# Kernel optimization log

Hardware: AMD Instinct MI355X
Metric: run time of the kernel (lower is better)

The kernel has to match this reference:

```python
import jax, jax.numpy as jnp
import numpy as np

E = 1024
H = 16
D = E // H  # head_dim = 64


def setup_inputs() -> dict:
    key = jax.random.key(0)
    k_x, k_w1, k_b1, k_w2, k_b2 = jax.random.split(key, 5)
    s = 1.0 / np.sqrt(E)
    return {
        "x": jax.random.normal(k_x, (2, 2048, E), dtype=jnp.float32),
        "qkv_w": jax.random.uniform(k_w1, (3 * E, E), jnp.float32, -s, s),
        "qkv_b": jax.random.uniform(k_b1, (3 * E,), jnp.float32, -s, s),
        "out_w": jax.random.uniform(k_w2, (E, E), jnp.float32, -s, s),
        "out_b": jax.random.uniform(k_b2, (E,), jnp.float32, -s, s),
    }


def reference(x, qkv_w, qkv_b, out_w, out_b):
    B, T, _ = x.shape
    # qkv projection (torch Linear: x @ W.T + b)
    qkv = x @ qkv_w.T + qkv_b  # [B, T, 3E]
    q, k, v = jnp.split(qkv, 3, axis=-1)
    # [B, T, E] -> [B, H, T, D]
    def to_heads(t):
        return t.reshape(B, T, H, D).transpose(0, 2, 1, 3)
    q, k, v = to_heads(q), to_heads(k), to_heads(v)
    scale = 1.0 / np.sqrt(D).astype(np.float32)
    scores = jnp.einsum("bhqd,bhkd->bhqk", q, k) * scale  # [B, H, T, T]
    attn = jax.nn.softmax(scores, axis=-1)
    # dropout is identity in eval mode
    out = jnp.einsum("bhqk,bhkd->bhqd", attn, v)  # [B, H, T, D]
    out = out.transpose(0, 2, 1, 3).reshape(B, T, E)
    return out @ out_w.T + out_b
```

## Files before the change

### kernel.cpp

```cpp
#include <hip/hip_runtime.h>

#define TT 2048
#define BB 2
#define EE 1024
#define HH 16
#define DD 64
#define E3 3072
#define NTOK 4096

typedef unsigned short u16;
typedef _Float16 __attribute__((ext_vector_type(8))) half8;
typedef __attribute__((ext_vector_type(4))) float f32x4;

__device__ __forceinline__ unsigned f2h(float f) {
    union { _Float16 h; u16 u; } v; v.h = (_Float16)f; return (unsigned)v.u;
}

__device__ __forceinline__ void async_ld16(const u16* g, const u16* l) {
    auto gp = reinterpret_cast<const __attribute__((address_space(1))) unsigned*>(
        reinterpret_cast<uintptr_t>(g));
    auto lp = reinterpret_cast<__attribute__((address_space(3))) unsigned*>(
        reinterpret_cast<uintptr_t>(l));
    __builtin_amdgcn_global_load_lds(gp, lp, 16, 0, 0);
}

__global__ __launch_bounds__(256) void split3(
    const float* __restrict__ x, const float* __restrict__ w1,
    const float* __restrict__ w2,
    u16* __restrict__ xh, u16* __restrict__ w1h, u16* __restrict__ w2h)
{
    const int N1 = (NTOK * EE) / 4;
    const int N2 = N1 + (E3 * EE) / 4;
    int i = blockIdx.x * 256 + threadIdx.x;
    const float* src; u16* dst; int j;
    if (i < N1)      { src = x;  dst = xh;  j = i; }
    else if (i < N2) { src = w1; dst = w1h; j = i - N1; }
    else             { src = w2; dst = w2h; j = i - N2; }
    float4 v = ((const float4*)src)[j];
    *(uint2*)&dst[(size_t)j * 4] = make_uint2(
        f2h(v.x) | (f2h(v.y) << 16), f2h(v.z) | (f2h(v.w) << 16));
}

__global__ __launch_bounds__(256) void vtrans(
    const u16* __restrict__ qkv, u16* __restrict__ vt)
{
    __shared__ u16 L[64][72];
    const int tid = threadIdx.x;
    const int t0 = blockIdx.x * 64;
    const int h  = blockIdx.y;
    const int b  = blockIdx.z;
    const int row = tid >> 2;
    const int c16 = (tid & 3) << 4;

    const u16* src = qkv + (size_t)(b * TT + t0 + row) * E3 + 2 * EE + h * DD + c16;
    *(uint4*)&L[row][c16]     = *(const uint4*)src;
    *(uint4*)&L[row][c16 + 8] = *(const uint4*)(src + 8);
    __syncthreads();

    union { uint4 u[2]; u16 s[16]; } P;
#pragma unroll
    for (int j = 0; j < 16; ++j) P.s[j] = L[c16 + j][row];
    u16* dst = vt + ((size_t)(b * HH + h) * DD + row) * TT + t0 + c16;
    *(uint4*)dst       = P.u[0];
    *(uint4*)(dst + 8) = P.u[1];
}

template <int WMT, bool ALO, bool F16OUT>
__global__ __launch_bounds__(256) void gemm_f16(
    const u16* __restrict__ Ahg, const u16* __restrict__ Alg,
    const u16* __restrict__ Whg,
    const float* __restrict__ bias, void* __restrict__ Cout, int M, int N)
{
    constexpr int BM = WMT * 32;
    constexpr int AHALF = BM / 64;
    __shared__ u16 sAh[BM * 32];
    __shared__ u16 sAl[ALO ? BM * 32 : 64];
    __shared__ u16 sBh[128 * 32];

    const int tid  = threadIdx.x;
    const int lane = tid & 63;
    const int wave = tid >> 6;
    const int quad = lane >> 4;
    const int l16  = lane & 15;
    const int wm = wave >> 1, wn = wave & 1;
    const int m0 = blockIdx.y * BM;
    const int n0 = blockIdx.x * 128;

    const u16* agh[AHALF]; const u16* agl[AHALF]; int aldw[AHALF];
#pragma unroll
    for (int h = 0; h < AHALF; ++h) {
        int s = h * 256 + tid;
        int row = s >> 2, k8p = s & 3;
        int k8 = k8p ^ ((row >> 1) & 3);
        agh[h] = Ahg + (size_t)(m0 + row) * EE + k8 * 8;
        agl[h] = ALO ? Alg + (size_t)(m0 + row) * EE + k8 * 8 : nullptr;
        aldw[h] = (h * 256 + wave * 64) * 8;
    }
    const u16* bgh[2]; int bldw[2];
#pragma unroll
    for (int h = 0; h < 2; ++h) {
        int s = h * 256 + tid;
        int row = s >> 2, k8p = s & 3;
        int k8 = k8p ^ ((row >> 1) & 3);
        bgh[h] = Whg + (size_t)(n0 + row) * EE + k8 * 8;
        bldw[h] = (h * 256 + wave * 64) * 8;
    }

    int aoff[WMT], boff[4];
#pragma unroll
    for (int mt = 0; mt < WMT; ++mt) {
        int r = wm * (WMT * 16) + mt * 16 + l16;
        aoff[mt] = r * 32 + (quad ^ ((r >> 1) & 3)) * 8;
    }
#pragma unroll
    for (int nt = 0; nt < 4; ++nt) {
        int r = wn * 64 + nt * 16 + l16;
        boff[nt] = r * 32 + (quad ^ ((r >> 1) & 3)) * 8;
    }

    f32x4 acc[WMT][4];
#pragma unroll
    for (int mt = 0; mt < WMT; ++mt)
#pragma unroll
        for (int nt = 0; nt < 4; ++nt) acc[mt][nt] = (f32x4){0.f, 0.f, 0.f, 0.f};

    for (int k0 = 0; k0 < EE; k0 += 32) {
        __syncthreads();
#pragma unroll
        for (int h = 0; h < AHALF; ++h) {
            async_ld16(agh[h] + k0, sAh + aldw[h]);
            if (ALO) async_ld16(agl[h] + k0, sAl + aldw[h]);
        }
#pragma unroll
        for (int h = 0; h < 2; ++h)
            async_ld16(bgh[h] + k0, sBh + bldw[h]);
        __syncthreads();

        half8 fah[WMT], fal[WMT], fbh[4];
#pragma unroll
        for (int mt = 0; mt < WMT; ++mt) {
            fah[mt] = *(const half8*)&sAh[aoff[mt]];
            if (ALO) fal[mt] = *(const half8*)&sAl[aoff[mt]];
        }
#pragma unroll
        for (int nt = 0; nt < 4; ++nt)
            fbh[nt] = *(const half8*)&sBh[boff[nt]];
#pragma unroll
        for (int mt = 0; mt < WMT; ++mt)
#pragma unroll
            for (int nt = 0; nt < 4; ++nt) {
                f32x4 c = acc[mt][nt];
                if (ALO)
                    c = __builtin_amdgcn_mfma_f32_16x16x32_f16(fal[mt], fbh[nt], c, 0, 0, 0);
                c = __builtin_amdgcn_mfma_f32_16x16x32_f16(fah[mt], fbh[nt], c, 0, 0, 0);
                acc[mt][nt] = c;
            }
    }

    float bv[4];
#pragma unroll
    for (int nt = 0; nt < 4; ++nt) bv[nt] = bias[n0 + wn * 64 + nt * 16 + l16];
#pragma unroll
    for (int mt = 0; mt < WMT; ++mt)
#pragma unroll
        for (int nt = 0; nt < 4; ++nt)
#pragma unroll
            for (int r = 0; r < 4; ++r) {
                int rg = m0 + wm * (WMT * 16) + mt * 16 + quad * 4 + r;
                int cg = n0 + wn * 64 + nt * 16 + l16;
                float v = acc[mt][nt][r] + bv[nt];
                if (F16OUT) ((u16*)Cout)[(size_t)rg * N + cg] = (u16)f2h(v);
                else        ((float*)Cout)[(size_t)rg * N + cg] = v;
            }
}

__global__ __launch_bounds__(256, 3) void attn_mfma(
    const u16* __restrict__ qkv, const u16* __restrict__ vt,
    u16* __restrict__ obuf)
{
    __shared__ u16 KB[2][64][64];
    __shared__ u16 VB[2][64][64];
    __shared__ u16 QP[128][64];

    const int tid  = threadIdx.x;
    const int wave = tid >> 6;
    const int lane = tid & 63;
    const int quad = lane >> 4;
    const int l16  = lane & 15;

    const int q0 = blockIdx.x * 128;
    const int hh = blockIdx.y;
    const int b  = blockIdx.z;
    const float C1 = 0.18033688011112042f;

    const int srow = tid >> 3;
    const int schk = tid & 7;
    const int ldsw = wave * 512;

#pragma unroll
    for (int p = 0; p < 4; ++p) {
        int row = p * 32 + srow;
        const u16* qg = qkv + (size_t)(b * TT + q0 + row) * E3 + hh * DD
                        + ((schk ^ (row & 7)) << 3);
        async_ld16(qg, &QP[0][0] + p * 2048 + ldsw);
    }
#pragma unroll
    for (int p = 0; p < 2; ++p) {
        int row = p * 32 + srow;
        int sw8 = (schk ^ (row & 7)) << 3;
        async_ld16(qkv + (size_t)(b * TT + row) * E3 + EE + hh * DD + sw8,
                   &KB[0][0][0] + p * 2048 + ldsw);
        async_ld16(vt + ((size_t)(b * HH + hh) * DD + row) * TT + sw8,
                   &VB[0][0][0] + p * 2048 + ldsw);
    }
    __syncthreads();

    half8 qb[2][2];
#pragma unroll
    for (int qt = 0; qt < 2; ++qt) {
        int row = wave * 32 + qt * 16 + l16;
#pragma unroll
        for (int ks = 0; ks < 2; ++ks)
            qb[qt][ks] = *(const half8*)&QP[row][((ks * 4 + quad) ^ (row & 7)) << 3];
    }

    float l_i[2] = {0.f, 0.f};
    f32x4 o[4][2];
#pragma unroll
    for (int dt = 0; dt < 4; ++dt)
#pragma unroll
        for (int qt = 0; qt < 2; ++qt) o[dt][qt] = (f32x4){0.f, 0.f, 0.f, 0.f};

    int cur = 0;
    for (int kt = 0; kt < TT; kt += 64, cur ^= 1) {
        const int ktn = (kt + 64) & (TT - 1);
#pragma unroll
        for (int p = 0; p < 2; ++p) {
            int row = p * 32 + srow;
            int sw8 = (schk ^ (row & 7)) << 3;
            async_ld16(qkv + (size_t)(b * TT + ktn + row) * E3 + EE + hh * DD + sw8,
                       &KB[cur ^ 1][0][0] + p * 2048 + ldsw);
            async_ld16(vt + ((size_t)(b * HH + hh) * DD + row) * TT + ktn + sw8,
                       &VB[cur ^ 1][0][0] + p * 2048 + ldsw);
        }

        f32x4 s[2][4];
#pragma unroll
        for (int qt = 0; qt < 2; ++qt)
#pragma unroll
            for (int nt = 0; nt < 4; ++nt) s[qt][nt] = (f32x4){0.f, 0.f, 0.f, 0.f};
#pragma unroll
        for (int nt = 0; nt < 4; ++nt) {
            int r0 = nt * 16 + l16;
            half8 kf0 = *(const half8*)&KB[cur][r0][((quad)     ^ (r0 & 7)) << 3];
            half8 kf1 = *(const half8*)&KB[cur][r0][((4 + quad) ^ (r0 & 7)) << 3];
#pragma unroll
            for (int qt = 0; qt < 2; ++qt) {
                s[qt][nt] = __builtin_amdgcn_mfma_f32_16x16x32_f16(kf0, qb[qt][0], s[qt][nt], 0, 0, 0);
                s[qt][nt] = __builtin_amdgcn_mfma_f32_16x16x32_f16(kf1, qb[qt][1], s[qt][nt], 0, 0, 0);
            }
        }

#pragma unroll
        for (int qt = 0; qt < 2; ++qt) {
            int prow = wave * 32 + qt * 16 + l16;
            float rs = 0.f;
#pragma unroll
            for (int nt = 0; nt < 4; ++nt) {
                unsigned ph[4];
#pragma unroll
                for (int r = 0; r < 4; ++r) {
                    float pj = __builtin_amdgcn_exp2f(s[qt][nt][r] * C1);
                    rs += pj;
                    ph[r] = f2h(pj);
                }
                int phys = (nt * 2 + (quad >> 1)) ^ (prow & 7);
                *(uint2*)&QP[prow][phys * 8 + ((quad & 1) << 2)] =
                    make_uint2(ph[0] | (ph[1] << 16), ph[2] | (ph[3] << 16));
            }
            l_i[qt] += rs;
        }

#pragma unroll
        for (int ks = 0; ks < 2; ++ks) {
            half8 pf[2];
#pragma unroll
            for (int qt = 0; qt < 2; ++qt) {
                int prow = wave * 32 + qt * 16 + l16;
                pf[qt] = *(const half8*)&QP[prow][((ks * 4 + quad) ^ (prow & 7)) << 3];
            }
#pragma unroll
            for (int dt = 0; dt < 4; ++dt) {
                int vr = dt * 16 + l16;
                half8 vf = *(const half8*)&VB[cur][vr][((ks * 4 + quad) ^ (vr & 7)) << 3];
#pragma unroll
                for (int qt = 0; qt < 2; ++qt)
                    o[dt][qt] = __builtin_amdgcn_mfma_f32_16x16x32_f16(vf, pf[qt], o[dt][qt], 0, 0, 0);
            }
        }

        __syncthreads();
    }

    float inv[2];
#pragma unroll
    for (int qt = 0; qt < 2; ++qt) {
        float l = l_i[qt];
        l += __shfl_xor(l, 16, 64);
        l += __shfl_xor(l, 32, 64);
        inv[qt] = 1.f / l;
    }
#pragma unroll
    for (int qt = 0; qt < 2; ++qt) {
        size_t base = (size_t)(b * TT + q0 + wave * 32 + qt * 16 + l16) * EE + hh * DD;
#pragma unroll
        for (int dt = 0; dt < 4; ++dt) {
            unsigned hv[4];
#pragma unroll
            for (int r = 0; r < 4; ++r) hv[r] = f2h(o[dt][qt][r] * inv[qt]);
            *(uint2*)&obuf[base + dt * 16 + quad * 4] =
                make_uint2(hv[0] | (hv[1] << 16), hv[2] | (hv[3] << 16));
        }
    }
}

extern "C" void kernel_launch(void* const* d_in, const int* in_sizes, int n_in,
                              void* d_out, int out_size, void* d_ws, size_t ws_size,
                              hipStream_t stream)
{
    const float* x     = (const float*)d_in[0];
    const float* qkv_w = (const float*)d_in[1];
    const float* qkv_b = (const float*)d_in[2];
    const float* out_w = (const float*)d_in[3];
    const float* out_b = (const float*)d_in[4];
    float* out = (float*)d_out;

    const size_t NX  = (size_t)NTOK * EE;
    const size_t NW1 = (size_t)E3 * EE;
    const size_t NW2 = (size_t)EE * EE;
    const size_t NQ  = (size_t)NTOK * E3;

    u16* ws   = (u16*)d_ws;
    u16* x_h  = ws;
    u16* w1h  = ws + NX;
    u16* w2h  = w1h + NW1;
    u16* qkvb = w2h + NW2;
    u16* vtb  = qkvb + NQ;

    split3<<<dim3((unsigned)((NX + NW1 + NW2) / 4 / 256)), 256, 0, stream>>>(
        x, qkv_w, out_w, x_h, w1h, w2h);

    gemm_f16<4, false, true><<<dim3(E3 / 128, NTOK / 128), 256, 0, stream>>>(
        x_h, nullptr, w1h, qkv_b, (void*)qkvb, NTOK, E3);

    vtrans<<<dim3(TT / 64, HH, BB), 256, 0, stream>>>(qkvb, vtb);

    attn_mfma<<<dim3(TT / 128, HH, BB), 256, 0, stream>>>(qkvb, vtb, x_h);

    gemm_f16<2, false, false><<<dim3(EE / 128, NTOK / 64), 256, 0, stream>>>(
        x_h, nullptr, w2h, out_b, (void*)out, NTOK, EE);
}
```

Measured before the change: 193.9 us.

## Widen GEMM K-tile to 64, fold softmax scale into Q, pack exp conversions

The GEMM kernel drops the unused split-precision A path and now stages a 64-wide K slice per iteration with an XOR swizzle, which halves the number of barrier-separated load rounds. It also adds a launch bound for three blocks per CU. The QKV GEMM multiplies the Q columns by the softmax log2 scale in its epilogue, so the attention loop no longer multiplies each score. The attention loop also starts each score MFMA chain from a zero constant and uses packed round-toward-zero fp16 conversion for probabilities. The larger LDS tile and the occupancy hint may change occupancy, and round-toward-zero slightly alters rounding of probabilities and Q.

```diff
diff --git a/kernel.cpp b/kernel.cpp
--- a/kernel.cpp
+++ b/kernel.cpp
@@ -10,10 +10,16 @@
 
 typedef unsigned short u16;
 typedef _Float16 __attribute__((ext_vector_type(8))) half8;
+typedef __fp16 __attribute__((ext_vector_type(2))) fp16x2;
 typedef __attribute__((ext_vector_type(4))) float f32x4;
 
 __device__ __forceinline__ unsigned f2h(float f) {
     union { _Float16 h; u16 u; } v; v.h = (_Float16)f; return (unsigned)v.u;
+}
+__device__ __forceinline__ unsigned pkh(float a, float b) {
+    union { fp16x2 h; unsigned u; } v;
+    v.h = __builtin_amdgcn_cvt_pkrtz(a, b);
+    return v.u;
 }
 
 __device__ __forceinline__ void async_ld16(const u16* g, const u16* l) {
@@ -65,17 +71,15 @@
     *(uint4*)(dst + 8) = P.u[1];
 }
 
-template <int WMT, bool ALO, bool F16OUT>
-__global__ __launch_bounds__(256) void gemm_f16(
-    const u16* __restrict__ Ahg, const u16* __restrict__ Alg,
-    const u16* __restrict__ Whg,
+template <int WMT, bool QSCALE, bool F16OUT>
+__global__ __launch_bounds__(256, 3) void gemm_f16(
+    const u16* __restrict__ Ag, const u16* __restrict__ Wg,
     const float* __restrict__ bias, void* __restrict__ Cout, int M, int N)
 {
     constexpr int BM = WMT * 32;
-    constexpr int AHALF = BM / 64;
-    __shared__ u16 sAh[BM * 32];
-    __shared__ u16 sAl[ALO ? BM * 32 : 64];
-    __shared__ u16 sBh[128 * 32];
+    constexpr int APASS = BM / 32;
+    __shared__ u16 sA[BM * 64];
+    __shared__ u16 sB[128 * 64];
 
     const int tid  = threadIdx.x;
     const int lane = tid & 63;
@@ -86,36 +90,22 @@
     const int m0 = blockIdx.y * BM;
     const int n0 = blockIdx.x * 128;
 
-    const u16* agh[AHALF]; const u16* agl[AHALF]; int aldw[AHALF];
-#pragma unroll
-    for (int h = 0; h < AHALF; ++h) {
-        int s = h * 256 + tid;
-        int row = s >> 2, k8p = s & 3;
-        int k8 = k8p ^ ((row >> 1) & 3);
-        agh[h] = Ahg + (size_t)(m0 + row) * EE + k8 * 8;
-        agl[h] = ALO ? Alg + (size_t)(m0 + row) * EE + k8 * 8 : nullptr;
-        aldw[h] = (h * 256 + wave * 64) * 8;
-    }
-    const u16* bgh[2]; int bldw[2];
-#pragma unroll
-    for (int h = 0; h < 2; ++h) {
-        int s = h * 256 + tid;
-        int row = s >> 2, k8p = s & 3;
-        int k8 = k8p ^ ((row >> 1) & 3);
-        bgh[h] = Whg + (size_t)(n0 + row) * EE + k8 * 8;
-        bldw[h] = (h * 256 + wave * 64) * 8;
-    }
-
-    int aoff[WMT], boff[4];
-#pragma unroll
-    for (int mt = 0; mt < WMT; ++mt) {
-        int r = wm * (WMT * 16) + mt * 16 + l16;
-        aoff[mt] = r * 32 + (quad ^ ((r >> 1) & 3)) * 8;
-    }
-#pragma unroll
-    for (int nt = 0; nt < 4; ++nt) {
-        int r = wn * 64 + nt * 16 + l16;
-        boff[nt] = r * 32 + (quad ^ ((r >> 1) & 3)) * 8;
+    const int srow = tid >> 3;
+    const int schk = tid & 7;
+
+    const u16* ag[APASS]; int aldw[APASS];
+#pragma unroll
+    for (int p = 0; p < APASS; ++p) {
+        int row = p * 32 + srow;
+        ag[p] = Ag + (size_t)(m0 + row) * EE + ((schk ^ (row & 7)) << 3);
+        aldw[p] = (p * 256 + wave * 64) * 8;
+    }
+    const u16* bg[4]; int bldw[4];
+#pragma unroll
+    for (int p = 0; p < 4; ++p) {
+        int row = p * 32 + srow;
+        bg[p] = Wg + (size_t)(n0 + row) * EE + ((schk ^ (row & 7)) << 3);
+        bldw[p] = (p * 256 + wave * 64) * 8;
     }
 
     f32x4 acc[WMT][4];
@@ -124,39 +114,40 @@
 #pragma unroll
         for (int nt = 0; nt < 4; ++nt) acc[mt][nt] = (f32x4){0.f, 0.f, 0.f, 0.f};
 
-    for (int k0 = 0; k0 < EE; k0 += 32) {
+    for (int k0 = 0; k0 < EE; k0 += 64) {
         __syncthreads();
 #pragma unroll
-        for (int h = 0; h < AHALF; ++h) {
-            async_ld16(agh[h] + k0, sAh + aldw[h]);
-            if (ALO) async_ld16(agl[h] + k0, sAl + aldw[h]);
-        }
-#pragma unroll
-        for (int h = 0; h < 2; ++h)
-            async_ld16(bgh[h] + k0, sBh + bldw[h]);
+        for (int p = 0; p < APASS; ++p) async_ld16(ag[p] + k0, sA + aldw[p]);
+#pragma unroll
+        for (int p = 0; p < 4; ++p)    async_ld16(bg[p] + k0, sB + bldw[p]);
         __syncthreads();
 
-        half8 fah[WMT], fal[WMT], fbh[4];
+        half8 fa[WMT][2], fb[4][2];
 #pragma unroll
         for (int mt = 0; mt < WMT; ++mt) {
-            fah[mt] = *(const half8*)&sAh[aoff[mt]];
-            if (ALO) fal[mt] = *(const half8*)&sAl[aoff[mt]];
-        }
-#pragma unroll
-        for (int nt = 0; nt < 4; ++nt)
-            fbh[nt] = *(const half8*)&sBh[boff[nt]];
-#pragma unroll
-        for (int mt = 0; mt < WMT; ++mt)
-#pragma unroll
-            for (int nt = 0; nt < 4; ++nt) {
-                f32x4 c = acc[mt][nt];
-                if (ALO)
-                    c = __builtin_amdgcn_mfma_f32_16x16x32_f16(fal[mt], fbh[nt], c, 0, 0, 0);
-                c = __builtin_amdgcn_mfma_f32_16x16x32_f16(fah[mt], fbh[nt], c, 0, 0, 0);
-                acc[mt][nt] = c;
-            }
-    }
-
+            int r = wm * (WMT * 16) + mt * 16 + l16;
+#pragma unroll
+            for (int ks = 0; ks < 2; ++ks)
+                fa[mt][ks] = *(const half8*)&sA[r * 64 + (((ks * 4 + quad) ^ (r & 7)) << 3)];
+        }
+#pragma unroll
+        for (int nt = 0; nt < 4; ++nt) {
+            int r = wn * 64 + nt * 16 + l16;
+#pragma unroll
+            for (int ks = 0; ks < 2; ++ks)
+                fb[nt][ks] = *(const half8*)&sB[r * 64 + (((ks * 4 + quad) ^ (r & 7)) << 3)];
+        }
+#pragma unroll
+        for (int ks = 0; ks < 2; ++ks)
+#pragma unroll
+            for (int mt = 0; mt < WMT; ++mt)
+#pragma unroll
+                for (int nt = 0; nt < 4; ++nt)
+                    acc[mt][nt] = __builtin_amdgcn_mfma_f32_16x16x32_f16(
+                        fa[mt][ks], fb[nt][ks], acc[mt][nt], 0, 0, 0);
+    }
+
+    const float scale = (QSCALE && n0 < EE) ? 0.18033688011112042f : 1.0f;
     float bv[4];
 #pragma unroll
     for (int nt = 0; nt < 4; ++nt) bv[nt] = bias[n0 + wn * 64 + nt * 16 + l16];
@@ -168,7 +159,7 @@
             for (int r = 0; r < 4; ++r) {
                 int rg = m0 + wm * (WMT * 16) + mt * 16 + quad * 4 + r;
                 int cg = n0 + wn * 64 + nt * 16 + l16;
-                float v = acc[mt][nt][r] + bv[nt];
+                float v = (acc[mt][nt][r] + bv[nt]) * scale;
                 if (F16OUT) ((u16*)Cout)[(size_t)rg * N + cg] = (u16)f2h(v);
                 else        ((float*)Cout)[(size_t)rg * N + cg] = v;
             }
@@ -191,7 +182,6 @@
     const int q0 = blockIdx.x * 128;
     const int hh = blockIdx.y;
     const int b  = blockIdx.z;
-    const float C1 = 0.18033688011112042f;
 
     const int srow = tid >> 3;
     const int schk = tid & 7;
@@ -224,6 +214,7 @@
             qb[qt][ks] = *(const half8*)&QP[row][((ks * 4 + quad) ^ (row & 7)) << 3];
     }
 
+    const f32x4 Z = {0.f, 0.f, 0.f, 0.f};
     float l_i[2] = {0.f, 0.f};
     f32x4 o[4][2];
 #pragma unroll
@@ -246,39 +237,34 @@
 
         f32x4 s[2][4];
 #pragma unroll
-        for (int qt = 0; qt < 2; ++qt)
-#pragma unroll
-            for (int nt = 0; nt < 4; ++nt) s[qt][nt] = (f32x4){0.f, 0.f, 0.f, 0.f};
-#pragma unroll
         for (int nt = 0; nt < 4; ++nt) {
             int r0 = nt * 16 + l16;
             half8 kf0 = *(const half8*)&KB[cur][r0][((quad)     ^ (r0 & 7)) << 3];
             half8 kf1 = *(const half8*)&KB[cur][r0][((4 + quad) ^ (r0 & 7)) << 3];
 #pragma unroll
             for (int qt = 0; qt < 2; ++qt) {
-                s[qt][nt] = __builtin_amdgcn_mfma_f32_16x16x32_f16(kf0, qb[qt][0], s[qt][nt], 0, 0, 0);
-                s[qt][nt] = __builtin_amdgcn_mfma_f32_16x16x32_f16(kf1, qb[qt][1], s[qt][nt], 0, 0, 0);
+                f32x4 t = __builtin_amdgcn_mfma_f32_16x16x32_f16(kf0, qb[qt][0], Z, 0, 0, 0);
+                s[qt][nt] = __builtin_amdgcn_mfma_f32_16x16x32_f16(kf1, qb[qt][1], t, 0, 0, 0);
             }
         }
 
 #pragma unroll
         for (int qt = 0; qt < 2; ++qt) {
             int prow = wave * 32 + qt * 16 + l16;
-            float rs = 0.f;
+            float rs0 = 0.f, rs1 = 0.f;
 #pragma unroll
             for (int nt = 0; nt < 4; ++nt) {
-                unsigned ph[4];
-#pragma unroll
-                for (int r = 0; r < 4; ++r) {
-                    float pj = __builtin_amdgcn_exp2f(s[qt][nt][r] * C1);
-                    rs += pj;
-                    ph[r] = f2h(pj);
-                }
+                float p0 = __builtin_amdgcn_exp2f(s[qt][nt][0]);
+                float p1 = __builtin_amdgcn_exp2f(s[qt][nt][1]);
+                float p2 = __builtin_amdgcn_exp2f(s[qt][nt][2]);
+                float p3 = __builtin_amdgcn_exp2f(s[qt][nt][3]);
+                rs0 += p0 + p1;
+                rs1 += p2 + p3;
                 int phys = (nt * 2 + (quad >> 1)) ^ (prow & 7);
                 *(uint2*)&QP[prow][phys * 8 + ((quad & 1) << 2)] =
-                    make_uint2(ph[0] | (ph[1] << 16), ph[2] | (ph[3] << 16));
-            }
-            l_i[qt] += rs;
+                    make_uint2(pkh(p0, p1), pkh(p2, p3));
+            }
+            l_i[qt] += rs0 + rs1;
         }
 
 #pragma unroll
@@ -350,13 +336,13 @@
     split3<<<dim3((unsigned)((NX + NW1 + NW2) / 4 / 256)), 256, 0, stream>>>(
         x, qkv_w, out_w, x_h, w1h, w2h);
 
-    gemm_f16<4, false, true><<<dim3(E3 / 128, NTOK / 128), 256, 0, stream>>>(
-        x_h, nullptr, w1h, qkv_b, (void*)qkvb, NTOK, E3);
+    gemm_f16<4, true, true><<<dim3(E3 / 128, NTOK / 128), 256, 0, stream>>>(
+        x_h, w1h, qkv_b, (void*)qkvb, NTOK, E3);
 
     vtrans<<<dim3(TT / 64, HH, BB), 256, 0, stream>>>(qkvb, vtb);
 
     attn_mfma<<<dim3(TT / 128, HH, BB), 256, 0, stream>>>(qkvb, vtb, x_h);
 
     gemm_f16<2, false, false><<<dim3(EE / 128, NTOK / 64), 256, 0, stream>>>(
-        x_h, nullptr, w2h, out_b, (void*)out, NTOK, EE);
-}
+        x_h, w2h, out_b, (void*)out, NTOK, EE);
+}
```

Result: faster. 189.4 us (-2.3%).
